# Kernel tuning notes

Measured on AMD Instinct MI355X. Metric: run time of the kernel, lower is better.

Reference implementation:

```python
import jax, jax.numpy as jnp
import numpy as np

B, S, D, F, E, TOP_K = 4, 2048, 1024, 4096, 8, 2


def setup_inputs() -> dict:
    key = jax.random.key(0)
    ks = jax.random.split(key, 6)
    sd = 1.0 / np.sqrt(D)
    sf = 1.0 / np.sqrt(F)
    return {
        "x": jax.random.normal(ks[0], (B, S, D), dtype=jnp.float32),
        "router_w": jax.random.normal(ks[1], (E, D), dtype=jnp.float32) * sd,
        "router_b": jnp.zeros((E,), dtype=jnp.float32),
        "w1": jax.random.normal(ks[2], (E, F, D), dtype=jnp.float32) * sd,  # Linear(d_model->d_ff) weight [out,in]
        "w2": jax.random.normal(ks[3], (E, D, F), dtype=jnp.float32) * sf,  # Linear(d_ff->d_model)
        "w3": jax.random.normal(ks[4], (E, F, D), dtype=jnp.float32) * sd,
    }


def reference(x, router_w, router_b, w1, w2, w3):
    # Router: softmax over experts, then top-k with renormalized gates.
    logits = jnp.einsum("bsd,ed->bse", x, router_w) + router_b          # [B,S,E]
    probs = jax.nn.softmax(logits, axis=-1)
    topk_p, topk_i = jax.lax.top_k(probs, TOP_K)                         # [B,S,K]
    topk_p = topk_p / jnp.sum(topk_p, axis=-1, keepdims=True)
    # Per-token combine weight for each expert (0 if not selected).
    combine = jnp.sum(jax.nn.one_hot(topk_i, E, dtype=x.dtype) * topk_p[..., None], axis=-2)  # [B,S,E]

    # Note: expert(x*mask)*mask == expert(x)*mask since SwiGLU(0)=0 (no bias).
    out = jnp.zeros_like(x)
    for e in range(E):  # small fixed expert count
        h = jax.nn.silu(jnp.einsum("bsd,fd->bsf", x, w1[e])) * jnp.einsum("bsd,fd->bsf", x, w3[e])
        out = out + combine[..., e:e + 1] * jnp.einsum("bsf,df->bsd", h, w2[e])
    return out
```

## Files before the change

### kernel.cpp

```cpp
#include <hip/hip_runtime.h>
#include <hip/hip_fp16.h>


#define NTOK 8192
#define D_ 1024
#define F_ 4096
#define E_ 8
#define SLOT_CAP 18432

using half8 = __attribute__((ext_vector_type(8))) _Float16;
using half4 = __attribute__((ext_vector_type(4))) _Float16;
using f32x4 = __attribute__((ext_vector_type(4))) float;

__device__ __forceinline__ void gload16(const void* g, void* l) {
  __builtin_amdgcn_global_load_lds((const __attribute__((address_space(1))) void*)g,
                                   (__attribute__((address_space(3))) void*)l, 16, 0, 0);
}

__global__ __launch_bounds__(256) void cvt_weights_kernel(
    const float* __restrict__ w1, const float* __restrict__ w3, const float* __restrict__ w2,
    _Float16* __restrict__ w13, _Float16* __restrict__ w2h) {
  int b = blockIdx.x;
  if (b < 4096) {
    for (int i = b * 256 + threadIdx.x; i < E_ * F_ * D_ / 4; i += 4096 * 256) {
      int d4 = i & 255;
      int row = i >> 8;
      int e = row >> 12, f = row & 4095;
      size_t vbase = ((size_t)e << 13) | ((size_t)(f >> 4) << 5) | (size_t)(f & 15);
      float4 v1 = ((const float4*)w1)[i];
      float4 v3 = ((const float4*)w3)[i];
      half4 h1, h3;
      h1.x = (_Float16)v1.x; h1.y = (_Float16)v1.y; h1.z = (_Float16)v1.z; h1.w = (_Float16)v1.w;
      h3.x = (_Float16)v3.x; h3.y = (_Float16)v3.y; h3.z = (_Float16)v3.z; h3.w = (_Float16)v3.w;
      ((half4*)w13)[vbase * 256 + d4] = h1;
      ((half4*)w13)[(vbase + 16) * 256 + d4] = h3;
    }
  } else {
    for (int i = (b - 4096) * 256 + threadIdx.x; i < E_ * D_ * F_ / 4; i += 4096 * 256) {
      float4 v = ((const float4*)w2)[i];
      half4 h;
      h.x = (_Float16)v.x; h.y = (_Float16)v.y; h.z = (_Float16)v.z; h.w = (_Float16)v.w;
      ((half4*)w2h)[i] = h;
    }
  }
}

__global__ __launch_bounds__(256) void router_kernel(
    const float* __restrict__ x, const float* __restrict__ rw, const float* __restrict__ rbias,
    _Float16* __restrict__ x16, int* __restrict__ tok_e, float* __restrict__ tok_g) {
  int wv = threadIdx.x >> 6, lane = threadIdx.x & 63;
  int t = blockIdx.x * 4 + wv;
  const float4* xr = (const float4*)(x + (size_t)t * D_);
  float acc[E_];
#pragma unroll
  for (int e = 0; e < E_; ++e) acc[e] = 0.f;
  for (int i = lane; i < D_ / 4; i += 64) {
    float4 xv = xr[i];
    half4 hx;
    hx.x = (_Float16)xv.x; hx.y = (_Float16)xv.y; hx.z = (_Float16)xv.z; hx.w = (_Float16)xv.w;
    ((half4*)(x16 + (size_t)t * D_))[i] = hx;
#pragma unroll
    for (int e = 0; e < E_; ++e) {
      float4 wv4 = ((const float4*)(rw + (size_t)e * D_))[i];
      acc[e] += xv.x * wv4.x + xv.y * wv4.y + xv.z * wv4.z + xv.w * wv4.w;
    }
  }
#pragma unroll
  for (int e = 0; e < E_; ++e) {
#pragma unroll
    for (int off = 32; off > 0; off >>= 1) acc[e] += __shfl_down(acc[e], off);
  }
  if (lane == 0) {
    float p[E_], mx = -1e30f;
#pragma unroll
    for (int e = 0; e < E_; ++e) { p[e] = acc[e] + rbias[e]; mx = fmaxf(mx, p[e]); }
#pragma unroll
    for (int e = 0; e < E_; ++e) p[e] = expf(p[e] - mx);
    int i0 = 0;
#pragma unroll
    for (int e = 1; e < E_; ++e) if (p[e] > p[i0]) i0 = e;
    int i1 = (i0 == 0) ? 1 : 0;
#pragma unroll
    for (int e = 0; e < E_; ++e) if (e != i0 && p[e] > p[i1]) i1 = e;
    float s = p[i0] + p[i1];
    tok_e[t * 2] = i0; tok_e[t * 2 + 1] = i1;
    tok_g[t * 2] = p[i0] / s; tok_g[t * 2 + 1] = p[i1] / s;
  }
}

__global__ __launch_bounds__(1024) void scatter_kernel(
    const int* __restrict__ tok_e, int* __restrict__ slot_token,
    int* __restrict__ slot_of, int* __restrict__ offs) {
  __shared__ int wcnt[16][E_];
  int t = threadIdx.x, lane = t & 63, wv = t >> 6;

  int total[E_];
#pragma unroll
  for (int e = 0; e < E_; ++e) total[e] = 0;
  for (int c = 0; c < NTOK * 2; c += 1024) {
    int ei = tok_e[c + t];
#pragma unroll
    for (int e = 0; e < E_; ++e) {
      unsigned long long m = __ballot(ei == e);
      if (lane == 0) wcnt[wv][e] = __popcll(m);
    }
    __syncthreads();
#pragma unroll
    for (int e = 0; e < E_; ++e) {
      int s = 0;
#pragma unroll
      for (int w2 = 0; w2 < 16; ++w2) s += wcnt[w2][e];
      total[e] += s;
    }
    __syncthreads();
  }
  int base[E_ + 1];
  {
    int o = 0;
#pragma unroll
    for (int e = 0; e < E_; ++e) { base[e] = o; o += ((total[e] + 255) >> 8) << 8; }
    base[E_] = o;
  }
  if (t <= E_) offs[t] = base[t];
#pragma unroll
  for (int e = 0; e < E_; ++e)
    for (int p = base[e] + total[e] + t; p < base[e + 1]; p += 1024) slot_token[p] = 0;

  int run[E_];
#pragma unroll
  for (int e = 0; e < E_; ++e) run[e] = 0;
  for (int c = 0; c < NTOK * 2; c += 1024) {
    int ei = tok_e[c + t];
    int rank = 0;
#pragma unroll
    for (int e = 0; e < E_; ++e) {
      unsigned long long m = __ballot(ei == e);
      if (lane == 0) wcnt[wv][e] = __popcll(m);
      if (ei == e) rank = __popcll(m & ((1ULL << lane) - 1ULL));
    }
    __syncthreads();
    int mybase = 0, wbase = 0;
    int tot[E_];
#pragma unroll
    for (int e = 0; e < E_; ++e) {
      int s = 0;
#pragma unroll
      for (int w2 = 0; w2 < 16; ++w2) {
        int v = wcnt[w2][e];
        if (e == ei && w2 < wv) wbase += v;
        s += v;
      }
      tot[e] = s;
      if (e == ei) mybase = base[e] + run[e];
    }
    int pos = mybase + wbase + rank;
    slot_token[pos] = (c + t) >> 1;
    slot_of[c + t] = pos;
#pragma unroll
    for (int e = 0; e < E_; ++e) run[e] += tot[e];
    __syncthreads();
  }
}

template <int MODE, int ORD, int KSPLIT, int KD, int NBN, int RPX, int BEROWS>
__global__ __launch_bounds__(512, 2) void moe_gemm_kernel(
    const _Float16* __restrict__ Amat, const _Float16* __restrict__ Bmat,
    const int* __restrict__ slot_token, const int* __restrict__ offs,
    void* __restrict__ outp, void* __restrict__ outp2) {
  constexpr int BM = 256;
  constexpr int MROW = 8;
  constexpr int AH = BM * 32;
  constexpr int BUFH = (BM + 256) * 32;
  constexpr int KL = KD / KSPLIT;
  constexpr int NT = KL / 32;
  __shared__ _Float16 lds[4 * BUFH];

  int id = blockIdx.x;
  int xcd = id & 7, idx = id >> 3;
  int vr, nb;
  if constexpr (ORD == 0) {
    int band = idx / (8 * NBN);
    int i2 = idx - band * (8 * NBN);
    int rib = (RPX - band * 8) < 8 ? (RPX - band * 8) : 8;
    nb = i2 / rib;
    vr = xcd * RPX + band * 8 + (i2 - nb * rib);
  } else {
    nb = idx % NBN;
    vr = xcd * RPX + idx / NBN;
  }
  int rb = vr, ks = 0;
  if constexpr (KSPLIT == 2) { rb = vr >> 1; ks = vr & 1; }
  int row0 = rb * BM;
  if (row0 >= offs[E_]) return;
  int e = 0;
#pragma unroll
  for (int i = 1; i < E_; ++i) if (row0 >= offs[i]) e = i;
  int koff = ks * KL;

  int t = threadIdx.x, l = t & 63, w = t >> 6;
  int wr = w >> 2, wc = w & 3;
  int srow = t >> 2;
  int gsrc8 = ((l & 3) ^ ((l >> 3) & 3)) * 8;

  const _Float16* aP0;
  const _Float16* aP1;
  if constexpr (MODE == 0) {
    int tk0 = slot_token[row0 + srow];
    int tk1 = slot_token[row0 + srow + 128];
    aP0 = Amat + (size_t)tk0 * KD + koff + gsrc8;
    aP1 = Amat + (size_t)tk1 * KD + koff + gsrc8;
  } else {
    aP0 = Amat + (size_t)(row0 + srow) * KD + koff + gsrc8;
    aP1 = Amat + (size_t)(row0 + srow + 128) * KD + koff + gsrc8;
  }
  const _Float16* b0P =
      Bmat + ((size_t)e * BEROWS + (size_t)nb * 256 + srow) * KD + koff + gsrc8;
  const _Float16* b1P = b0P + (size_t)128 * KD;

  int fr = l & 15, kg = l >> 4;
  int swz8 = (kg ^ ((fr >> 1) & 3)) * 8;
  const int rA = (wr * 128 + fr) * 32 + swz8;
  const int rB = AH + (wc * 64 + fr) * 32 + swz8;

  half8 aF[4];
  half8 bF[4];
  f32x4 acc[MROW][4];
#pragma unroll
  for (int m = 0; m < MROW; ++m)
#pragma unroll
    for (int n = 0; n < 4; ++n) acc[m][n] = (f32x4){0.f, 0.f, 0.f, 0.f};

#pragma unroll
  for (int tt = 0; tt < 3; ++tt) {
    gload16(aP0 + tt * 32, &lds[tt * BUFH + w * 512]);
    gload16(aP1 + tt * 32, &lds[tt * BUFH + 4096 + w * 512]);
    gload16(b0P + tt * 32, &lds[tt * BUFH + AH + w * 512]);
    gload16(b1P + tt * 32, &lds[tt * BUFH + AH + 4096 + w * 512]);
  }
  asm volatile("s_waitcnt vmcnt(8)" ::: "memory");
  __builtin_amdgcn_s_barrier();
  __builtin_amdgcn_sched_barrier(0);
  aP0 += 96; aP1 += 96; b0P += 96; b1P += 96;

#define MF16(BASE)                                                           \
  _Pragma("unroll") for (int mi = 0; mi < 4; ++mi)                           \
  _Pragma("unroll") for (int ni = 0; ni < 4; ++ni)                           \
      acc[(BASE) + mi][ni] = __builtin_amdgcn_mfma_f32_16x16x32_f16(         \
          aF[mi], bF[ni], acc[(BASE) + mi][ni], 0, 0, 0);

#define STEPP(U, PRE, WN)                                                         \
  {                                                                               \
    constexpr int bi_ = (U) & 3;                                                  \
    constexpr int bs_ = ((U) + 3) & 3;                                            \
    const _Float16* cb_ = &lds[bi_ * BUFH];                                       \
    if (PRE) {                                                                    \
      gload16(aP0 + (U) * 32, &lds[bs_ * BUFH + w * 512]);                        \
      gload16(aP1 + (U) * 32, &lds[bs_ * BUFH + 4096 + w * 512]);                 \
    }                                                                             \
    aF[0] = *(const half8*)(cb_ + rA);                                            \
    aF[1] = *(const half8*)(cb_ + rA + 512);                                      \
    aF[2] = *(const half8*)(cb_ + rA + 1024);                                     \
    aF[3] = *(const half8*)(cb_ + rA + 1536);                                     \
    bF[0] = *(const half8*)(cb_ + rB);                                            \
    bF[1] = *(const half8*)(cb_ + rB + 512);                                      \
    bF[2] = *(const half8*)(cb_ + rB + 1024);                                     \
    bF[3] = *(const half8*)(cb_ + rB + 1536);                                     \
    __builtin_amdgcn_sched_barrier(0);                                            \
    __builtin_amdgcn_s_barrier();                                                 \
    asm volatile("s_waitcnt lgkmcnt(0)" ::: "memory");                            \
    __builtin_amdgcn_sched_barrier(0);                                            \
    __builtin_amdgcn_s_setprio(1);                                                \
    MF16(0)                                                                       \
    __builtin_amdgcn_s_setprio(0);                                                \
    __builtin_amdgcn_sched_barrier(0);                                            \
    __builtin_amdgcn_s_barrier();                                                 \
    if (PRE) {                                                                    \
      gload16(b0P + (U) * 32, &lds[bs_ * BUFH + AH + w * 512]);                   \
      gload16(b1P + (U) * 32, &lds[bs_ * BUFH + AH + 4096 + w * 512]);            \
    }                                                                             \
    aF[0] = *(const half8*)(cb_ + rA + 2048);                                     \
    aF[1] = *(const half8*)(cb_ + rA + 2560);                                     \
    aF[2] = *(const half8*)(cb_ + rA + 3072);                                     \
    aF[3] = *(const half8*)(cb_ + rA + 3584);                                     \
    __builtin_amdgcn_sched_barrier(0);                                            \
    __builtin_amdgcn_s_barrier();                                                 \
    asm volatile("s_waitcnt lgkmcnt(0)" ::: "memory");                            \
    __builtin_amdgcn_sched_barrier(0);                                            \
    __builtin_amdgcn_s_setprio(1);                                                \
    MF16(4)                                                                       \
    __builtin_amdgcn_s_setprio(0);                                                \
    if ((WN) >= 0) {                                                              \
      asm volatile("s_waitcnt vmcnt(%0)" ::"i"((WN) >= 0 ? (WN) : 0) : "memory"); \
      __builtin_amdgcn_sched_barrier(0);                                          \
      __builtin_amdgcn_s_barrier();                                               \
      __builtin_amdgcn_sched_barrier(0);                                          \
    }                                                                             \
  }

  for (int j4 = 0; j4 < NT - 4; j4 += 4) {
    STEPP(0, true, 8)
    STEPP(1, true, 8)
    STEPP(2, true, 8)
    STEPP(3, true, 8)
    aP0 += 128; aP1 += 128; b0P += 128; b1P += 128;
  }
  STEPP(0, true, 8)
  STEPP(1, false, 4)
  STEPP(2, false, 0)
  STEPP(3, false, -1)
#undef STEPP
#undef MF16

  int q4 = kg * 4;
  if constexpr (MODE == 0) {
    _Float16* hb = (_Float16*)outp;
#pragma unroll
    for (int mi = 0; mi < MROW; ++mi) {
      size_t rbase = (size_t)(row0 + wr * 128 + mi * 16 + q4);
#pragma unroll
      for (int p = 0; p < 2; ++p) {
        int fc = nb * 128 + (wc * 2 + p) * 16 + fr;
#pragma unroll
        for (int i = 0; i < 4; ++i) {
          float gv = acc[mi][2 * p][i];
          float hv = gv / (1.f + __expf(-gv)) * acc[mi][2 * p + 1][i];
          hb[(rbase + i) * (size_t)F_ + fc] = (_Float16)hv;
        }
      }
    }
  } else {
    float* yb = (float*)(ks == 0 ? outp : outp2);
#pragma unroll
    for (int mi = 0; mi < MROW; ++mi) {
      size_t rbase = (size_t)(row0 + wr * 128 + mi * 16 + q4);
#pragma unroll
      for (int ni = 0; ni < 4; ++ni) {
        int col = nb * 256 + wc * 64 + ni * 16 + fr;
#pragma unroll
        for (int i = 0; i < 4; ++i)
          yb[(rbase + i) * (size_t)D_ + col] = acc[mi][ni][i];
      }
    }
  }
}

__global__ __launch_bounds__(256) void combine_kernel(
    const float* __restrict__ ya, const float* __restrict__ yb2,
    const int* __restrict__ slot_of, const float* __restrict__ tok_g,
    float* __restrict__ out) {
  int t = blockIdx.x, i = threadIdx.x;
  int s0 = slot_of[t * 2], s1 = slot_of[t * 2 + 1];
  float g0 = tok_g[t * 2], g1 = tok_g[t * 2 + 1];
  float4 a0 = ((const float4*)(ya + (size_t)s0 * D_))[i];
  float4 a1 = ((const float4*)(yb2 + (size_t)s0 * D_))[i];
  float4 b0 = ((const float4*)(ya + (size_t)s1 * D_))[i];
  float4 b1 = ((const float4*)(yb2 + (size_t)s1 * D_))[i];
  float4 r;
  r.x = g0 * (a0.x + a1.x) + g1 * (b0.x + b1.x);
  r.y = g0 * (a0.y + a1.y) + g1 * (b0.y + b1.y);
  r.z = g0 * (a0.z + a1.z) + g1 * (b0.z + b1.z);
  r.w = g0 * (a0.w + a1.w) + g1 * (b0.w + b1.w);
  ((float4*)(out + (size_t)t * D_))[i] = r;
}

extern "C" void kernel_launch(void* const* d_in, const int* in_sizes, int n_in,
                              void* d_out, int out_size, void* d_ws, size_t ws_size,
                              hipStream_t stream) {
  const float* x  = (const float*)d_in[0];
  const float* rw = (const float*)d_in[1];
  const float* rbc = (const float*)d_in[2];
  const float* w1 = (const float*)d_in[3];
  const float* w2 = (const float*)d_in[4];
  const float* w3 = (const float*)d_in[5];
  float* out = (float*)d_out;

  char* ws = (char*)d_ws;
  size_t off = 0;
  auto take = [&](size_t bytes) {
    char* p = ws + off;
    off = (off + bytes + 255) & ~(size_t)255;
    return p;
  };
  _Float16* x16 = (_Float16*)take((size_t)NTOK * D_ * 2);
  _Float16* w13 = (_Float16*)take((size_t)E_ * 2 * F_ * D_ * 2);
  _Float16* w2h = (_Float16*)take((size_t)E_ * D_ * F_ * 2);
  _Float16* hbuf = (_Float16*)take((size_t)SLOT_CAP * F_ * 2);
  float* ybuf = (float*)take((size_t)SLOT_CAP * D_ * 4);
  int* slot_token = (int*)take((size_t)SLOT_CAP * 4);
  int* tok_e = (int*)take((size_t)NTOK * 2 * 4);
  float* tok_g = (float*)take((size_t)NTOK * 2 * 4);
  int* slot_of = (int*)take((size_t)NTOK * 2 * 4);
  int* offs = (int*)take((E_ + 1) * 4);
  float* ybuf2 = (float*)w13;

  cvt_weights_kernel<<<8192, 256, 0, stream>>>(w1, w3, w2, w13, w2h);
  router_kernel<<<NTOK / 4, 256, 0, stream>>>(x, rw, rbc, x16, tok_e, tok_g);
  scatter_kernel<<<1, 1024, 0, stream>>>(tok_e, slot_token, slot_of, offs);
  moe_gemm_kernel<0, 0, 1, 1024, 32, 9, 8192><<<2304, 512, 0, stream>>>(
      x16, w13, slot_token, offs, (void*)hbuf, nullptr);
  moe_gemm_kernel<1, 1, 2, 4096, 4, 18, 1024><<<576, 512, 0, stream>>>(
      hbuf, w2h, slot_token, offs, (void*)ybuf, (void*)ybuf2);
  combine_kernel<<<NTOK, 256, 0, stream>>>(ybuf, ybuf2, slot_of, tok_g, out);
}
```

Measured before the change: 737.4 us.

## Shrink MoE GEMM tile, load B fragments from global, merge prep kernels

The expert GEMM tile shrinks from 256 to 128 rows. The B operand is no longer staged in LDS: each wave reads its B fragments straight from global memory into registers. LDS now holds only A, which drops several barriers and lets launch bounds rise to four blocks per CU, with grids doubled to match. The weight-conversion and router kernels are also merged into one prep launch to save a launch. In exchange, B reuse across waves and row tiles is lost, so global B traffic roughly quadruples. The B loads also sit unprefetched on the critical path of each MFMA step.

```diff
diff --git a/kernel.cpp b/kernel.cpp
--- a/kernel.cpp
+++ b/kernel.cpp
@@ -17,9 +17,11 @@
                                    (__attribute__((address_space(3))) void*)l, 16, 0, 0);
 }
 
-__global__ __launch_bounds__(256) void cvt_weights_kernel(
+__global__ __launch_bounds__(256) void prep_kernel(
     const float* __restrict__ w1, const float* __restrict__ w3, const float* __restrict__ w2,
-    _Float16* __restrict__ w13, _Float16* __restrict__ w2h) {
+    const float* __restrict__ x, const float* __restrict__ rw, const float* __restrict__ rbias,
+    _Float16* __restrict__ w13, _Float16* __restrict__ w2h, _Float16* __restrict__ x16,
+    int* __restrict__ tok_e, float* __restrict__ tok_g) {
   int b = blockIdx.x;
   if (b < 4096) {
     for (int i = b * 256 + threadIdx.x; i < E_ * F_ * D_ / 4; i += 4096 * 256) {
@@ -35,56 +37,52 @@
       ((half4*)w13)[vbase * 256 + d4] = h1;
       ((half4*)w13)[(vbase + 16) * 256 + d4] = h3;
     }
-  } else {
+  } else if (b < 8192) {
     for (int i = (b - 4096) * 256 + threadIdx.x; i < E_ * D_ * F_ / 4; i += 4096 * 256) {
       float4 v = ((const float4*)w2)[i];
       half4 h;
       h.x = (_Float16)v.x; h.y = (_Float16)v.y; h.z = (_Float16)v.z; h.w = (_Float16)v.w;
       ((half4*)w2h)[i] = h;
     }
-  }
-}
-
-__global__ __launch_bounds__(256) void router_kernel(
-    const float* __restrict__ x, const float* __restrict__ rw, const float* __restrict__ rbias,
-    _Float16* __restrict__ x16, int* __restrict__ tok_e, float* __restrict__ tok_g) {
-  int wv = threadIdx.x >> 6, lane = threadIdx.x & 63;
-  int t = blockIdx.x * 4 + wv;
-  const float4* xr = (const float4*)(x + (size_t)t * D_);
-  float acc[E_];
-#pragma unroll
-  for (int e = 0; e < E_; ++e) acc[e] = 0.f;
-  for (int i = lane; i < D_ / 4; i += 64) {
-    float4 xv = xr[i];
-    half4 hx;
-    hx.x = (_Float16)xv.x; hx.y = (_Float16)xv.y; hx.z = (_Float16)xv.z; hx.w = (_Float16)xv.w;
-    ((half4*)(x16 + (size_t)t * D_))[i] = hx;
-#pragma unroll
-    for (int e = 0; e < E_; ++e) {
-      float4 wv4 = ((const float4*)(rw + (size_t)e * D_))[i];
-      acc[e] += xv.x * wv4.x + xv.y * wv4.y + xv.z * wv4.z + xv.w * wv4.w;
-    }
-  }
-#pragma unroll
-  for (int e = 0; e < E_; ++e) {
-#pragma unroll
-    for (int off = 32; off > 0; off >>= 1) acc[e] += __shfl_down(acc[e], off);
-  }
-  if (lane == 0) {
-    float p[E_], mx = -1e30f;
-#pragma unroll
-    for (int e = 0; e < E_; ++e) { p[e] = acc[e] + rbias[e]; mx = fmaxf(mx, p[e]); }
-#pragma unroll
-    for (int e = 0; e < E_; ++e) p[e] = expf(p[e] - mx);
-    int i0 = 0;
-#pragma unroll
-    for (int e = 1; e < E_; ++e) if (p[e] > p[i0]) i0 = e;
-    int i1 = (i0 == 0) ? 1 : 0;
-#pragma unroll
-    for (int e = 0; e < E_; ++e) if (e != i0 && p[e] > p[i1]) i1 = e;
-    float s = p[i0] + p[i1];
-    tok_e[t * 2] = i0; tok_e[t * 2 + 1] = i1;
-    tok_g[t * 2] = p[i0] / s; tok_g[t * 2 + 1] = p[i1] / s;
+  } else {
+    int wv = threadIdx.x >> 6, lane = threadIdx.x & 63;
+    int t = (b - 8192) * 4 + wv;
+    const float4* xr = (const float4*)(x + (size_t)t * D_);
+    float acc[E_];
+#pragma unroll
+    for (int e = 0; e < E_; ++e) acc[e] = 0.f;
+    for (int i = lane; i < D_ / 4; i += 64) {
+      float4 xv = xr[i];
+      half4 hx;
+      hx.x = (_Float16)xv.x; hx.y = (_Float16)xv.y; hx.z = (_Float16)xv.z; hx.w = (_Float16)xv.w;
+      ((half4*)(x16 + (size_t)t * D_))[i] = hx;
+#pragma unroll
+      for (int e = 0; e < E_; ++e) {
+        float4 wv4 = ((const float4*)(rw + (size_t)e * D_))[i];
+        acc[e] += xv.x * wv4.x + xv.y * wv4.y + xv.z * wv4.z + xv.w * wv4.w;
+      }
+    }
+#pragma unroll
+    for (int e = 0; e < E_; ++e) {
+#pragma unroll
+      for (int off = 32; off > 0; off >>= 1) acc[e] += __shfl_down(acc[e], off);
+    }
+    if (lane == 0) {
+      float p[E_], mx = -1e30f;
+#pragma unroll
+      for (int e = 0; e < E_; ++e) { p[e] = acc[e] + rbias[e]; mx = fmaxf(mx, p[e]); }
+#pragma unroll
+      for (int e = 0; e < E_; ++e) p[e] = expf(p[e] - mx);
+      int i0 = 0;
+#pragma unroll
+      for (int e = 1; e < E_; ++e) if (p[e] > p[i0]) i0 = e;
+      int i1 = (i0 == 0) ? 1 : 0;
+#pragma unroll
+      for (int e = 0; e < E_; ++e) if (e != i0 && p[e] > p[i1]) i1 = e;
+      float s = p[i0] + p[i1];
+      tok_e[t * 2] = i0; tok_e[t * 2 + 1] = i1;
+      tok_g[t * 2] = p[i0] / s; tok_g[t * 2 + 1] = p[i1] / s;
+    }
   }
 }
 
@@ -163,14 +161,13 @@
 }
 
 template <int MODE, int ORD, int KSPLIT, int KD, int NBN, int RPX, int BEROWS>
-__global__ __launch_bounds__(512, 2) void moe_gemm_kernel(
+__global__ __launch_bounds__(512, 4) void moe_gemm_kernel(
     const _Float16* __restrict__ Amat, const _Float16* __restrict__ Bmat,
     const int* __restrict__ slot_token, const int* __restrict__ offs,
     void* __restrict__ outp, void* __restrict__ outp2) {
-  constexpr int BM = 256;
-  constexpr int MROW = 8;
-  constexpr int AH = BM * 32;
-  constexpr int BUFH = (BM + 256) * 32;
+  constexpr int BM = 128;
+  constexpr int MROW = 4;
+  constexpr int BUFH = BM * 32;
   constexpr int KL = KD / KSPLIT;
   constexpr int NT = KL / 32;
   __shared__ _Float16 lds[4 * BUFH];
@@ -201,29 +198,22 @@
   int wr = w >> 2, wc = w & 3;
   int srow = t >> 2;
   int gsrc8 = ((l & 3) ^ ((l >> 3) & 3)) * 8;
-
-  const _Float16* aP0;
-  const _Float16* aP1;
+  int fr = l & 15, kg = l >> 4;
+
+  const _Float16* aP;
   if constexpr (MODE == 0) {
-    int tk0 = slot_token[row0 + srow];
-    int tk1 = slot_token[row0 + srow + 128];
-    aP0 = Amat + (size_t)tk0 * KD + koff + gsrc8;
-    aP1 = Amat + (size_t)tk1 * KD + koff + gsrc8;
+    int tk = slot_token[row0 + srow];
+    aP = Amat + (size_t)tk * KD + koff + gsrc8;
   } else {
-    aP0 = Amat + (size_t)(row0 + srow) * KD + koff + gsrc8;
-    aP1 = Amat + (size_t)(row0 + srow + 128) * KD + koff + gsrc8;
-  }
-  const _Float16* b0P =
-      Bmat + ((size_t)e * BEROWS + (size_t)nb * 256 + srow) * KD + koff + gsrc8;
-  const _Float16* b1P = b0P + (size_t)128 * KD;
-
-  int fr = l & 15, kg = l >> 4;
+    aP = Amat + (size_t)(row0 + srow) * KD + koff + gsrc8;
+  }
+  const _Float16* bP =
+      Bmat + ((size_t)e * BEROWS + (size_t)nb * 256 + wc * 64 + fr) * KD + koff + (size_t)kg * 8;
+
   int swz8 = (kg ^ ((fr >> 1) & 3)) * 8;
-  const int rA = (wr * 128 + fr) * 32 + swz8;
-  const int rB = AH + (wc * 64 + fr) * 32 + swz8;
-
-  half8 aF[4];
-  half8 bF[4];
+  const int rA = (wr * 64 + fr) * 32 + swz8;
+
+  half8 aF[4], bF[4];
   f32x4 acc[MROW][4];
 #pragma unroll
   for (int m = 0; m < MROW; ++m)
@@ -231,92 +221,58 @@
     for (int n = 0; n < 4; ++n) acc[m][n] = (f32x4){0.f, 0.f, 0.f, 0.f};
 
 #pragma unroll
-  for (int tt = 0; tt < 3; ++tt) {
-    gload16(aP0 + tt * 32, &lds[tt * BUFH + w * 512]);
-    gload16(aP1 + tt * 32, &lds[tt * BUFH + 4096 + w * 512]);
-    gload16(b0P + tt * 32, &lds[tt * BUFH + AH + w * 512]);
-    gload16(b1P + tt * 32, &lds[tt * BUFH + AH + 4096 + w * 512]);
-  }
-  asm volatile("s_waitcnt vmcnt(8)" ::: "memory");
+  for (int tt = 0; tt < 3; ++tt) gload16(aP + tt * 32, &lds[tt * BUFH + w * 512]);
+  asm volatile("s_waitcnt vmcnt(2)" ::: "memory");
   __builtin_amdgcn_s_barrier();
   __builtin_amdgcn_sched_barrier(0);
-  aP0 += 96; aP1 += 96; b0P += 96; b1P += 96;
-
-#define MF16(BASE)                                                           \
-  _Pragma("unroll") for (int mi = 0; mi < 4; ++mi)                           \
-  _Pragma("unroll") for (int ni = 0; ni < 4; ++ni)                           \
-      acc[(BASE) + mi][ni] = __builtin_amdgcn_mfma_f32_16x16x32_f16(         \
-          aF[mi], bF[ni], acc[(BASE) + mi][ni], 0, 0, 0);
-
-#define STEPP(U, PRE, WN)                                                         \
+  aP += 96;
+
+#define STEPP(U, PRE, FIN)                                                        \
   {                                                                               \
     constexpr int bi_ = (U) & 3;                                                  \
     constexpr int bs_ = ((U) + 3) & 3;                                            \
     const _Float16* cb_ = &lds[bi_ * BUFH];                                       \
-    if (PRE) {                                                                    \
-      gload16(aP0 + (U) * 32, &lds[bs_ * BUFH + w * 512]);                        \
-      gload16(aP1 + (U) * 32, &lds[bs_ * BUFH + 4096 + w * 512]);                 \
-    }                                                                             \
+    bF[0] = *(const half8*)(bP + (U) * 32);                                       \
+    bF[1] = *(const half8*)(bP + (U) * 32 + 16 * (size_t)KD);                     \
+    bF[2] = *(const half8*)(bP + (U) * 32 + 32 * (size_t)KD);                     \
+    bF[3] = *(const half8*)(bP + (U) * 32 + 48 * (size_t)KD);                     \
+    if (PRE) gload16(aP + (U) * 32, &lds[bs_ * BUFH + w * 512]);                  \
     aF[0] = *(const half8*)(cb_ + rA);                                            \
     aF[1] = *(const half8*)(cb_ + rA + 512);                                      \
     aF[2] = *(const half8*)(cb_ + rA + 1024);                                     \
     aF[3] = *(const half8*)(cb_ + rA + 1536);                                     \
-    bF[0] = *(const half8*)(cb_ + rB);                                            \
-    bF[1] = *(const half8*)(cb_ + rB + 512);                                      \
-    bF[2] = *(const half8*)(cb_ + rB + 1024);                                     \
-    bF[3] = *(const half8*)(cb_ + rB + 1536);                                     \
-    __builtin_amdgcn_sched_barrier(0);                                            \
-    __builtin_amdgcn_s_barrier();                                                 \
-    asm volatile("s_waitcnt lgkmcnt(0)" ::: "memory");                            \
-    __builtin_amdgcn_sched_barrier(0);                                            \
     __builtin_amdgcn_s_setprio(1);                                                \
-    MF16(0)                                                                       \
+    _Pragma("unroll") for (int mi = 0; mi < MROW; ++mi)                           \
+    _Pragma("unroll") for (int ni = 0; ni < 4; ++ni)                              \
+        acc[mi][ni] = __builtin_amdgcn_mfma_f32_16x16x32_f16(aF[mi], bF[ni],      \
+                                                             acc[mi][ni], 0, 0, 0); \
     __builtin_amdgcn_s_setprio(0);                                                \
-    __builtin_amdgcn_sched_barrier(0);                                            \
-    __builtin_amdgcn_s_barrier();                                                 \
-    if (PRE) {                                                                    \
-      gload16(b0P + (U) * 32, &lds[bs_ * BUFH + AH + w * 512]);                   \
-      gload16(b1P + (U) * 32, &lds[bs_ * BUFH + AH + 4096 + w * 512]);            \
-    }                                                                             \
-    aF[0] = *(const half8*)(cb_ + rA + 2048);                                     \
-    aF[1] = *(const half8*)(cb_ + rA + 2560);                                     \
-    aF[2] = *(const half8*)(cb_ + rA + 3072);                                     \
-    aF[3] = *(const half8*)(cb_ + rA + 3584);                                     \
-    __builtin_amdgcn_sched_barrier(0);                                            \
-    __builtin_amdgcn_s_barrier();                                                 \
-    asm volatile("s_waitcnt lgkmcnt(0)" ::: "memory");                            \
-    __builtin_amdgcn_sched_barrier(0);                                            \
-    __builtin_amdgcn_s_setprio(1);                                                \
-    MF16(4)                                                                       \
-    __builtin_amdgcn_s_setprio(0);                                                \
-    if ((WN) >= 0) {                                                              \
-      asm volatile("s_waitcnt vmcnt(%0)" ::"i"((WN) >= 0 ? (WN) : 0) : "memory"); \
-      __builtin_amdgcn_sched_barrier(0);                                          \
+    if (!(FIN)) {                                                                 \
+      asm volatile("s_waitcnt vmcnt(1)" ::: "memory");                            \
       __builtin_amdgcn_s_barrier();                                               \
       __builtin_amdgcn_sched_barrier(0);                                          \
     }                                                                             \
   }
 
   for (int j4 = 0; j4 < NT - 4; j4 += 4) {
-    STEPP(0, true, 8)
-    STEPP(1, true, 8)
-    STEPP(2, true, 8)
-    STEPP(3, true, 8)
-    aP0 += 128; aP1 += 128; b0P += 128; b1P += 128;
-  }
-  STEPP(0, true, 8)
-  STEPP(1, false, 4)
-  STEPP(2, false, 0)
-  STEPP(3, false, -1)
+    STEPP(0, true, false)
+    STEPP(1, true, false)
+    STEPP(2, true, false)
+    STEPP(3, true, false)
+    aP += 128; bP += 128;
+  }
+  STEPP(0, true, false)
+  STEPP(1, false, false)
+  STEPP(2, false, false)
+  STEPP(3, false, true)
 #undef STEPP
-#undef MF16
 
   int q4 = kg * 4;
   if constexpr (MODE == 0) {
     _Float16* hb = (_Float16*)outp;
 #pragma unroll
     for (int mi = 0; mi < MROW; ++mi) {
-      size_t rbase = (size_t)(row0 + wr * 128 + mi * 16 + q4);
+      size_t rbase = (size_t)(row0 + wr * 64 + mi * 16 + q4);
 #pragma unroll
       for (int p = 0; p < 2; ++p) {
         int fc = nb * 128 + (wc * 2 + p) * 16 + fr;
@@ -332,7 +288,7 @@
     float* yb = (float*)(ks == 0 ? outp : outp2);
 #pragma unroll
     for (int mi = 0; mi < MROW; ++mi) {
-      size_t rbase = (size_t)(row0 + wr * 128 + mi * 16 + q4);
+      size_t rbase = (size_t)(row0 + wr * 64 + mi * 16 + q4);
 #pragma unroll
       for (int ni = 0; ni < 4; ++ni) {
         int col = nb * 256 + wc * 64 + ni * 16 + fr;
@@ -393,12 +349,11 @@
   int* offs = (int*)take((E_ + 1) * 4);
   float* ybuf2 = (float*)w13;
 
-  cvt_weights_kernel<<<8192, 256, 0, stream>>>(w1, w3, w2, w13, w2h);
-  router_kernel<<<NTOK / 4, 256, 0, stream>>>(x, rw, rbc, x16, tok_e, tok_g);
+  prep_kernel<<<10240, 256, 0, stream>>>(w1, w3, w2, x, rw, rbc, w13, w2h, x16, tok_e, tok_g);
   scatter_kernel<<<1, 1024, 0, stream>>>(tok_e, slot_token, slot_of, offs);
-  moe_gemm_kernel<0, 0, 1, 1024, 32, 9, 8192><<<2304, 512, 0, stream>>>(
+  moe_gemm_kernel<0, 0, 1, 1024, 32, 18, 8192><<<4608, 512, 0, stream>>>(
       x16, w13, slot_token, offs, (void*)hbuf, nullptr);
-  moe_gemm_kernel<1, 1, 2, 4096, 4, 18, 1024><<<576, 512, 0, stream>>>(
+  moe_gemm_kernel<1, 1, 2, 4096, 4, 36, 1024><<<1152, 512, 0, stream>>>(
       hbuf, w2h, slot_token, offs, (void*)ybuf, (void*)ybuf2);
   combine_kernel<<<NTOK, 256, 0, stream>>>(ybuf, ybuf2, slot_of, tok_g, out);
 }
```

Result: slower. 1.238 ms (+67.9%).
